# Optimization experiments

Hardware: AMD Instinct MI355X
Metric: run time of the kernel (lower is better)

The kernel has to match this reference:

```python
import jax, jax.numpy as jnp
import numpy as np

B, C, H, W, HEADS, S = 8, 512, 32, 32, 8, 77
CH = C // HEADS  # per-head channels = 64
GROUPS = 32      # GroupNorm32


def setup_inputs() -> dict:
    key = jax.random.key(0)
    ks = jax.random.split(key, 6)
    s = 0.02
    return {
        "x": jax.random.normal(ks[0], (B, C, H, W), jnp.float32),
        "encoder_out": jax.random.normal(ks[1], (B, C, S), jnp.float32),
        "capt_attn_mask": jax.random.bernoulli(ks[2], 0.9, (B, S)),
        "norm_scale": jnp.ones((C,), jnp.float32),
        "norm_bias": jnp.zeros((C,), jnp.float32),
        "qkv_w": jax.random.normal(ks[3], (3 * C, C), jnp.float32) * s,
        "qkv_b": jnp.zeros((3 * C,), jnp.float32),
        "ekv_w": jax.random.normal(ks[4], (2 * C, C), jnp.float32) * s,
        "ekv_b": jnp.zeros((2 * C,), jnp.float32),
        "proj_w": jax.random.normal(ks[5], (C, C), jnp.float32) * s,
        "proj_b": jnp.zeros((C,), jnp.float32),
    }


def reference(x, encoder_out, capt_attn_mask, norm_scale, norm_bias,
              qkv_w, qkv_b, ekv_w, ekv_b, proj_w, proj_b):
    b, c, h, w = x.shape
    T = h * w
    xf = x.reshape(b, c, T)

    # GroupNorm(32) in fp32 (GroupNorm32), affine
    xg = xf.reshape(b, GROUPS, c // GROUPS, T).astype(jnp.float32)
    mu = xg.mean(axis=(2, 3), keepdims=True)
    var = xg.var(axis=(2, 3), keepdims=True)
    nrm = ((xg - mu) * jax.lax.rsqrt(var + 1e-5)).reshape(b, c, T)
    nrm = nrm * norm_scale[None, :, None] + norm_bias[None, :, None]

    # 1x1 conv1d qkv projection: [b, 3c, T]
    qkv = jnp.einsum('oc,bct->bot', qkv_w, nrm) + qkv_b[None, :, None]
    qkv = qkv.reshape(b * HEADS, 3 * CH, T)
    q, k, v = jnp.split(qkv, 3, axis=1)  # each [b*heads, CH, T]

    # encoder kv: [b, 2c, S] -> [b*heads, 2*CH, S]
    ekv = jnp.einsum('oc,bcs->bos', ekv_w, encoder_out) + ekv_b[None, :, None]
    ekv = ekv.reshape(b * HEADS, 2 * CH, S)
    ek, ev = jnp.split(ekv, 2, axis=1)
    k = jnp.concatenate([ek, k], axis=-1)  # [b*heads, CH, S+T]
    v = jnp.concatenate([ev, v], axis=-1)

    scale = 1.0 / np.sqrt(np.sqrt(CH))
    wgt = jnp.einsum('bct,bcs->bts', q * scale, k * scale).astype(jnp.float32)

    # additive mask; torch.tile over dim0 is head-major (row i -> batch i % b),
    # faithfully reproduced; self-attn part (last T cols) is all-visible.
    addm_capt = jnp.where(jnp.tile(capt_attn_mask, (HEADS, 1)), 0.0, -10000.0)
    addm = jnp.concatenate(
        [addm_capt, jnp.zeros((b * HEADS, T), jnp.float32)], axis=1)[:, None, :]
    wgt = jax.nn.softmax(wgt + addm, axis=-1).astype(v.dtype)

    out = jnp.einsum('bts,bcs->bct', wgt, v)  # [b*heads, CH, T]
    out = out.reshape(b, c, T)
    out = jnp.einsum('oc,bct->bot', proj_w, out) + proj_b[None, :, None]
    return (xf + out).reshape(b, c, h, w)
```

## Files before the change

kernel.cpp:

```cpp
#include <hip/hip_runtime.h>
#include <math.h>

#define BB 8
#define TT 1024
#define SS 77

typedef short v8s __attribute__((ext_vector_type(8)));
typedef float v4f __attribute__((ext_vector_type(4)));
typedef unsigned short u16x4 __attribute__((ext_vector_type(4)));
typedef unsigned short u16x8 __attribute__((ext_vector_type(8)));
typedef unsigned short u16;

#define SCALEF 0.424660891f
#define MASKNEG (-14426.95f)

__device__ __forceinline__ u16 f2bf(float f) {
  unsigned u = __float_as_uint(f);
  u = (u + 0x7fffu + ((u >> 16) & 1u)) >> 16;
  return (u16)u;
}
__device__ __forceinline__ u16 hi16(float f) {
  return (u16)(__float_as_uint(f) >> 16);
}
__device__ __forceinline__ float bf2f(u16 u) {
  return __uint_as_float(((unsigned)u) << 16);
}
__device__ __forceinline__ void gl_lds16(const void* g, void* l) {
  __builtin_amdgcn_global_load_lds(
      (const __attribute__((address_space(1))) void*)g,
      (__attribute__((address_space(3))) void*)l, 16, 0, 0);
}

__global__ __launch_bounds__(256) void prep_gn_kernel(
    const float* __restrict__ x, const float* __restrict__ scale,
    const float* __restrict__ bias, u16* __restrict__ nrmT,
    const float* __restrict__ qkv_w, const float* __restrict__ ekv_w,
    const float* __restrict__ proj_w, const float* __restrict__ enc,
    const float* __restrict__ qkv_b, const float* __restrict__ ekv_b,
    u16* __restrict__ wQK, u16* __restrict__ wV, u16* __restrict__ wEK,
    u16* __restrict__ wEV, u16* __restrict__ projwb, u16* __restrict__ encT,
    float* __restrict__ bQK, float* __restrict__ bV,
    float* __restrict__ bEK, float* __restrict__ bEV) {
  __shared__ u16 Xs[16 * 1024];
  __shared__ float red[8];
  int blk = blockIdx.x, tid = threadIdx.x;

  if (blk < 256) {
    int bg = blk;
    int b = bg >> 5, g = bg & 31;
    const float4* x4 = (const float4*)(x + (size_t)bg * 16384);
    float s = 0.f, sq = 0.f;
#pragma unroll
    for (int i = 0; i < 16; ++i) {
      int idx = tid + 256 * i;
      float4 v = x4[idx];
      s += v.x + v.y + v.z + v.w;
      sq += v.x * v.x + v.y * v.y + v.z * v.z + v.w * v.w;
      int c = idx >> 8, t4 = (idx & 255) * 4;
      u16x4 o; o.x = f2bf(v.x); o.y = f2bf(v.y); o.z = f2bf(v.z); o.w = f2bf(v.w);
      *(u16x4*)(Xs + c * 1024 + t4) = o;
    }
#pragma unroll
    for (int off = 32; off > 0; off >>= 1) {
      s += __shfl_down(s, off, 64);
      sq += __shfl_down(sq, off, 64);
    }
    int wave = tid >> 6;
    if ((tid & 63) == 0) { red[wave] = s; red[wave + 4] = sq; }
    __syncthreads();
    float ts = red[0] + red[1] + red[2] + red[3];
    float tq = red[4] + red[5] + red[6] + red[7];
    float mu = ts * (1.0f / 16384.0f);
    float var = tq * (1.0f / 16384.0f) - mu * mu;
    float rs = rsqrtf(var + 1e-5f);
    float scv[16], biv[16];
#pragma unroll
    for (int c = 0; c < 16; ++c) {
      float ss = scale[g * 16 + c] * rs;
      scv[c] = ss;
      biv[c] = bias[g * 16 + c] - mu * ss;
    }
#pragma unroll
    for (int j = 0; j < 4; ++j) {
      int t = tid + 256 * j;
      u16x8 o0, o1;
#pragma unroll
      for (int c = 0; c < 8; ++c)  o0[c] = f2bf(bf2f(Xs[c * 1024 + t]) * scv[c] + biv[c]);
#pragma unroll
      for (int c = 8; c < 16; ++c) o1[c - 8] = f2bf(bf2f(Xs[c * 1024 + t]) * scv[c] + biv[c]);
      u16* dst = nrmT + ((size_t)b * 1024 + t) * 512 + g * 16;
      *(u16x8*)dst = o0;
      *(u16x8*)(dst + 8) = o1;
    }
    return;
  }

  int p = blk - 256;
  if (p < 512) {
    int idx = p * 256 + tid;
    int n = idx >> 7, c4 = (idx & 127) * 4;
    int which = n >> 9, h = (n >> 6) & 7, ch = n & 63;
    int src = h * 192 + which * 64 + ch;
    float4 v = *(const float4*)(qkv_w + (size_t)src * 512 + c4);
    u16x4 o; o.x = f2bf(v.x * SCALEF); o.y = f2bf(v.y * SCALEF);
    o.z = f2bf(v.z * SCALEF); o.w = f2bf(v.w * SCALEF);
    *(u16x4*)(wQK + (size_t)n * 512 + c4) = o;
  } else if (p < 768) {
    int idx = (p - 512) * 256 + tid;
    int n = idx >> 7, c4 = (idx & 127) * 4;
    int h = n >> 6, ch = n & 63;
    int src = h * 192 + 128 + ch;
    float4 v = *(const float4*)(qkv_w + (size_t)src * 512 + c4);
    u16x4 o; o.x = f2bf(v.x); o.y = f2bf(v.y); o.z = f2bf(v.z); o.w = f2bf(v.w);
    *(u16x4*)(wV + (size_t)n * 512 + c4) = o;
  } else if (p < 1024) {
    int idx = (p - 768) * 256 + tid;
    int n = idx >> 7, c4 = (idx & 127) * 4;
    int h = n >> 6, ch = n & 63;
    int src = h * 128 + ch;
    float4 v = *(const float4*)(ekv_w + (size_t)src * 512 + c4);
    u16x4 o; o.x = f2bf(v.x * SCALEF); o.y = f2bf(v.y * SCALEF);
    o.z = f2bf(v.z * SCALEF); o.w = f2bf(v.w * SCALEF);
    *(u16x4*)(wEK + (size_t)n * 512 + c4) = o;
  } else if (p < 1280) {
    int idx = (p - 1024) * 256 + tid;
    int n = idx >> 7, c4 = (idx & 127) * 4;
    int h = n >> 6, ch = n & 63;
    int src = h * 128 + 64 + ch;
    float4 v = *(const float4*)(ekv_w + (size_t)src * 512 + c4);
    u16x4 o; o.x = f2bf(v.x); o.y = f2bf(v.y); o.z = f2bf(v.z); o.w = f2bf(v.w);
    *(u16x4*)(wEV + (size_t)n * 512 + c4) = o;
  } else if (p < 1536) {
    int idx = (p - 1280) * 256 + tid;
    float4 v = ((const float4*)proj_w)[idx];
    u16x4 o; o.x = f2bf(v.x); o.y = f2bf(v.y); o.z = f2bf(v.z); o.w = f2bf(v.w);
    *(u16x4*)(projwb + (size_t)idx * 4) = o;
  } else if (p < 2048) {
    int idx = (p - 1536) * 256 + tid;
    int b = idx >> 14, rem = idx & 16383;
    int s = rem >> 7, c = (rem & 127) * 4;
    u16x4 o; o.x = 0; o.y = 0; o.z = 0; o.w = 0;
    if (s < SS) {
      const float* pp = enc + ((size_t)b * 512 + c) * SS + s;
      o.x = f2bf(pp[0]); o.y = f2bf(pp[SS]); o.z = f2bf(pp[2 * SS]); o.w = f2bf(pp[3 * SS]);
    }
    *(u16x4*)(encT + ((size_t)b * 128 + s) * 512 + c) = o;
  } else {
    for (int i = tid; i < 2560; i += 256) {
      if (i < 1024) {
        int which = i >> 9, h = (i >> 6) & 7, ch = i & 63;
        bQK[i] = qkv_b[h * 192 + which * 64 + ch] * SCALEF;
      } else if (i < 1536) {
        int j = i - 1024; int h = j >> 6, ch = j & 63;
        bV[j] = qkv_b[h * 192 + 128 + ch];
      } else if (i < 2048) {
        int j = i - 1536; int h = j >> 6, ch = j & 63;
        bEK[j] = ekv_b[h * 128 + ch] * SCALEF;
      } else {
        int j = i - 2048; int h = j >> 6, ch = j & 63;
        bEV[j] = ekv_b[h * 128 + 64 + ch];
      }
    }
  }
}

__global__ __launch_bounds__(256) void proj_all(
    const u16* __restrict__ nrmT, const u16* __restrict__ encT,
    const u16* __restrict__ wQK, const u16* __restrict__ wEK,
    const u16* __restrict__ wV, const u16* __restrict__ wEV,
    const float* __restrict__ bQK, const float* __restrict__ bEK,
    const float* __restrict__ bV, const float* __restrict__ bEV,
    u16* __restrict__ Qh, u16* __restrict__ Kfull, u16* __restrict__ Vfull) {
  __shared__ __align__(16) u16 SH[16384];
  u16* As = SH;
  u16* Bs = SH + 8192;

  int job = blockIdx.x, bz = blockIdx.y;
  int tid = threadIdx.x;
  int lane = tid & 63, w = tid >> 6;
  int lan15 = lane & 15, quad = lane >> 4;
  int wm = w >> 1, wn = w & 1;

  int mode, m0, n0;
  const u16 *Ap, *Bp;
  const float* bias;
  u16 *dA = nullptr, *dB = nullptr;
  int TrA = 0, offA = 0, TrB = 0, offB = 0;
  int coff = 0;

  if (job < 64) {
    mode = 3; m0 = (job >> 3) * 128; n0 = (job & 7) * 128;
    Ap = nrmT + (size_t)bz * 1024 * 512; Bp = wQK; bias = bQK;
    dA = Qh; TrA = 1024; offA = 0; dB = Kfull; TrB = 1152; offB = 128;
  } else if (job < 68) {
    mode = 3; m0 = 0; n0 = (job - 64) * 128;
    Ap = encT + (size_t)bz * 128 * 512; Bp = wEK; bias = bEK;
    dA = Kfull; TrA = 1152; offA = 0; dB = Kfull; TrB = 1152; offB = 0;
  } else if (job < 100) {
    int jj = job - 68; mode = 0; m0 = (jj >> 3) * 128; n0 = (jj & 7) * 128;
    Ap = wV; Bp = nrmT + (size_t)bz * 1024 * 512; bias = bV;
    coff = 128;
  } else {
    int jj = job - 100; mode = 0; m0 = jj * 128; n0 = 0;
    Ap = wEV; Bp = encT + (size_t)bz * 128 * 512; bias = bEV;
    coff = 0;
  }

  int srow = lane >> 3;
  int schunk = (lane & 7) ^ srow;
  const char* Ag = (const char*)(Ap + (size_t)(m0 + w * 32 + srow) * 512) + schunk * 16;
  const char* Bg = (const char*)(Bp + (size_t)(n0 + w * 32 + srow) * 512) + schunk * 16;
  char* Al = (char*)As + w * 4096;
  char* Bl = (char*)Bs + w * 4096;

  v4f acc[4][4] = {};

  for (int step = 0; step < 8; ++step) {
    __syncthreads();
    int kb = step * 128;
#pragma unroll
    for (int i = 0; i < 4; ++i) gl_lds16(Ag + kb + i * 8192, Al + i * 1024);
#pragma unroll
    for (int i = 0; i < 4; ++i) gl_lds16(Bg + kb + i * 8192, Bl + i * 1024);
    __syncthreads();

#pragma unroll
    for (int ksub = 0; ksub < 2; ++ksub) {
      int ch = ((ksub * 4 + quad) ^ (lan15 & 7)) * 16;
      v8s a[4], bf[4];
#pragma unroll
      for (int i = 0; i < 4; ++i)
        a[i] = *(const v8s*)((const char*)As + (wm * 64 + i * 16 + lan15) * 128 + ch);
#pragma unroll
      for (int j = 0; j < 4; ++j)
        bf[j] = *(const v8s*)((const char*)Bs + (wn * 64 + j * 16 + lan15) * 128 + ch);
#pragma unroll
      for (int i = 0; i < 4; ++i)
#pragma unroll
        for (int j = 0; j < 4; ++j)
          acc[i][j] = __builtin_amdgcn_mfma_f32_16x16x32_bf16(a[i], bf[j], acc[i][j], 0, 0, 0);
    }
  }

  if (mode == 3) {
    u16* Tr = SH;
    for (int ph = 0; ph < 2; ++ph) {
      __syncthreads();
      if (wn == ph) {
#pragma unroll
        for (int j = 0; j < 4; ++j) {
          int n = n0 + wn * 64 + j * 16 + lan15;
          float bv_ = bias[n];
#pragma unroll
          for (int i = 0; i < 4; ++i)
#pragma unroll
            for (int r = 0; r < 4; ++r)
              Tr[(wm * 64 + i * 16 + quad * 4 + r) * 72 + j * 16 + lan15] =
                  f2bf(acc[i][j][r] + bv_);
        }
      }
      __syncthreads();
      int nb = n0 + ph * 64;
      u16* dst = (nb < 512) ? dA : dB;
      int Trows = (nb < 512) ? TrA : TrB;
      int roff  = (nb < 512) ? offA : offB;
      int hh = (nb & 511) >> 6;
      int row = tid >> 1, seg = (tid & 1) * 32;
      u16* dp = dst + ((size_t)(bz * 8 + hh) * Trows + roff + m0 + row) * 64 + seg;
#pragma unroll
      for (int g = 0; g < 4; ++g)
        *(u16x8*)(dp + g * 8) = *(const u16x8*)(Tr + row * 72 + seg + g * 8);
    }
  } else {
    u16* Tr = SH;
    u16* Cb = Vfull + (size_t)bz * 512 * 1152;
    for (int ph = 0; ph < 2; ++ph) {
      __syncthreads();
      if (wn == ph) {
#pragma unroll
        for (int i = 0; i < 4; ++i) {
          int ob = wm * 64 + i * 16 + quad * 4;
#pragma unroll
          for (int r = 0; r < 4; ++r) {
            float bi = bias[m0 + ob + r];
#pragma unroll
            for (int j = 0; j < 4; ++j)
              Tr[(ob + r) * 72 + j * 16 + lan15] = f2bf(acc[i][j][r] + bi);
          }
        }
      }
      __syncthreads();
      int row = tid >> 1, seg = (tid & 1) * 32;
      u16* dp = Cb + (size_t)(m0 + row) * 1152 + coff + n0 + ph * 64 + seg;
#pragma unroll
      for (int g = 0; g < 4; ++g)
        *(u16x8*)(dp + g * 8) = *(const u16x8*)(Tr + row * 72 + seg + g * 8);
    }
  }
}

__global__ __launch_bounds__(256) void proj_out(
    const u16* __restrict__ A, const u16* __restrict__ B,
    const float* __restrict__ bias, const float* __restrict__ res,
    float* __restrict__ Cf) {
  __shared__ __align__(16) u16 SH[16384];
  u16* As = SH;
  u16* Bs = SH + 8192;

  int tid = threadIdx.x;
  int lane = tid & 63, w = tid >> 6;
  int lan15 = lane & 15, quad = lane >> 4;
  int wm = w >> 1, wn = w & 1;
  int m0 = blockIdx.y * 128, n0 = blockIdx.x * 128;
  int bz = blockIdx.z;
  const u16* Bb = B + (size_t)bz * 1024 * 512;

  int srow = lane >> 3;
  int schunk = (lane & 7) ^ srow;
  const char* Ag = (const char*)(A + (size_t)(m0 + w * 32 + srow) * 512) + schunk * 16;
  const char* Bg = (const char*)(Bb + (size_t)(n0 + w * 32 + srow) * 512) + schunk * 16;
  char* Al = (char*)As + w * 4096;
  char* Bl = (char*)Bs + w * 4096;

  v4f acc[4][4] = {};

  for (int step = 0; step < 8; ++step) {
    __syncthreads();
    int kb = step * 128;
#pragma unroll
    for (int i = 0; i < 4; ++i) gl_lds16(Ag + kb + i * 8192, Al + i * 1024);
#pragma unroll
    for (int i = 0; i < 4; ++i) gl_lds16(Bg + kb + i * 8192, Bl + i * 1024);
    __syncthreads();

#pragma unroll
    for (int ksub = 0; ksub < 2; ++ksub) {
      int ch = ((ksub * 4 + quad) ^ (lan15 & 7)) * 16;
      v8s a[4], bf[4];
#pragma unroll
      for (int i = 0; i < 4; ++i)
        a[i] = *(const v8s*)((const char*)As + (wm * 64 + i * 16 + lan15) * 128 + ch);
#pragma unroll
      for (int j = 0; j < 4; ++j)
        bf[j] = *(const v8s*)((const char*)Bs + (wn * 64 + j * 16 + lan15) * 128 + ch);
#pragma unroll
      for (int i = 0; i < 4; ++i)
#pragma unroll
        for (int j = 0; j < 4; ++j)
          acc[i][j] = __builtin_amdgcn_mfma_f32_16x16x32_bf16(a[i], bf[j], acc[i][j], 0, 0, 0);
    }
  }

  const float* rb = res + (size_t)bz * 512 * 1024;
  float* Cb = Cf + (size_t)bz * 512 * 1024;
#pragma unroll
  for (int i = 0; i < 4; ++i) {
    int ob = m0 + wm * 64 + i * 16 + quad * 4;
#pragma unroll
    for (int r = 0; r < 4; ++r) {
      int o = ob + r;
      float bi = bias[o];
#pragma unroll
      for (int j = 0; j < 4; ++j) {
        int n = n0 + wn * 64 + j * 16 + lan15;
        Cb[(size_t)o * 1024 + n] = acc[i][j][r] + bi + rb[(size_t)o * 1024 + n];
      }
    }
  }
}

#define AOFF_K 0
#define AOFF_V 24576
#define AOFF_P 49152
#define AOFF_AM 67584
#define ASMEM  68096

__global__ __launch_bounds__(512, 4) void attn_kernel(
    const u16* __restrict__ Qh, const u16* __restrict__ Kf,
    const u16* __restrict__ Vf, const int* __restrict__ mask,
    u16* __restrict__ attnT) {
  __shared__ __align__(16) unsigned char smem[ASMEM];
  float* AM = (float*)(smem + AOFF_AM);

  int bh = blockIdx.x, b = bh >> 3, h = bh & 7;
  int t0 = blockIdx.y * 128;
  int tid = threadIdx.x;
  int lane = tid & 63, w = tid >> 6;
  int lan15 = lane & 15, quad = lane >> 4;
  int r8 = lane >> 3, c8 = lane & 7;
  int swE = (c8 ^ r8) * 8;

  const u16* Qb = Qh + (size_t)bh * 1024 * 64;
  const u16* Kb = Kf + (size_t)bh * 1152 * 64;
  const u16* Vb = Vf + (size_t)bh * 64 * 1152;
  char* Pw = (char*)smem + AOFF_P + w * 2304;
  u16* Pu = (u16*)Pw;

  if (tid < 128)
    AM[tid] = (tid < SS) ? ((mask[h * SS + tid] != 0) ? 0.f : MASKNEG) : -1e30f;

#pragma unroll
  for (int i = 0; i < 2; ++i)
    gl_lds16(Qb + (size_t)(t0 + w * 16 + i * 8 + r8) * 64 + swE, Pw + i * 1024);
#pragma unroll
  for (int cc = 0; cc < 2; ++cc) {
    int row = w * 8;
    gl_lds16(Kb + (size_t)(cc * 64 + row + r8) * 64 + swE,
             (char*)smem + AOFF_K + cc * 8192 + row * 128);
    gl_lds16(Vb + (size_t)(row + r8) * 1152 + cc * 64 + swE,
             (char*)smem + AOFF_V + cc * 8192 + row * 128);
  }

  asm volatile("s_waitcnt vmcnt(4)" ::: "memory");
  __builtin_amdgcn_sched_barrier(0);

  v8s aq[2];
#pragma unroll
  for (int ks = 0; ks < 2; ++ks)
    aq[ks] = *(const v8s*)(Pw + lan15 * 128 +
                           (((ks * 4 + quad) ^ (lan15 & 7)) * 16));

  asm volatile("s_waitcnt vmcnt(2) lgkmcnt(0)" ::: "memory");
  __builtin_amdgcn_sched_barrier(0);
  __builtin_amdgcn_s_barrier();
  __builtin_amdgcn_sched_barrier(0);

  v4f O[4] = {};
  float lsum = 0.f;
  int cur = 0;

  for (int c = 0; c < 18; ++c) {
    if (c < 16) {
      int nb = cur + 2; if (nb >= 3) nb -= 3;
      int row = w * 8;
      gl_lds16(Kb + (size_t)((c + 2) * 64 + row + r8) * 64 + swE,
               (char*)smem + AOFF_K + nb * 8192 + row * 128);
      gl_lds16(Vb + (size_t)(row + r8) * 1152 + (c + 2) * 64 + swE,
               (char*)smem + AOFF_V + nb * 8192 + row * 128);
    }
    const char* Kc = (const char*)smem + AOFF_K + cur * 8192;
    const char* Vc = (const char*)smem + AOFF_V + cur * 8192;

    v4f ST[4] = {};
#pragma unroll
    for (int ks = 0; ks < 2; ++ks) {
      int cofs = ((ks * 4 + quad) ^ (lan15 & 7)) * 16;
      v8s bk[4];
#pragma unroll
      for (int nt = 0; nt < 4; ++nt)
        bk[nt] = *(const v8s*)(Kc + (nt * 16 + lan15) * 128 + cofs);
      __builtin_amdgcn_s_setprio(1);
#pragma unroll
      for (int nt = 0; nt < 4; ++nt)
        ST[nt] = __builtin_amdgcn_mfma_f32_16x16x32_bf16(bk[nt], aq[ks], ST[nt], 0, 0, 0);
      __builtin_amdgcn_s_setprio(0);
    }

    if (c < 2) {
#pragma unroll
      for (int nt = 0; nt < 4; ++nt)
#pragma unroll
        for (int r = 0; r < 4; ++r)
          ST[nt][r] += AM[c * 64 + nt * 16 + quad * 4 + r];
    }

#pragma unroll
    for (int nt = 0; nt < 4; ++nt) {
      float e0 = __builtin_amdgcn_exp2f(ST[nt][0]);
      float e1 = __builtin_amdgcn_exp2f(ST[nt][1]);
      float e2 = __builtin_amdgcn_exp2f(ST[nt][2]);
      float e3 = __builtin_amdgcn_exp2f(ST[nt][3]);
      u16x4 pk; pk.x = hi16(e0); pk.y = hi16(e1); pk.z = hi16(e2); pk.w = hi16(e3);
      *(u16x4*)&Pu[lan15 * 72 + nt * 16 + quad * 4] = pk;
      lsum += (e0 + e1) + (e2 + e3);
    }

#pragma unroll
    for (int ks = 0; ks < 2; ++ks) {
      int cofs = ((ks * 4 + quad) ^ (lan15 & 7)) * 16;
      v8s ap, bv[4];
      ap = *(const v8s*)(Pw + lan15 * 144 + ks * 64 + quad * 16);
#pragma unroll
      for (int nc = 0; nc < 4; ++nc)
        bv[nc] = *(const v8s*)(Vc + (nc * 16 + lan15) * 128 + cofs);
      __builtin_amdgcn_s_setprio(1);
#pragma unroll
      for (int nc = 0; nc < 4; ++nc)
        O[nc] = __builtin_amdgcn_mfma_f32_16x16x32_bf16(ap, bv[nc], O[nc], 0, 0, 0);
      __builtin_amdgcn_s_setprio(0);
    }

    if (c < 17) {
      if (c < 16) asm volatile("s_waitcnt vmcnt(2)" ::: "memory");
      else        asm volatile("s_waitcnt vmcnt(0)" ::: "memory");
      __builtin_amdgcn_sched_barrier(0);
      __builtin_amdgcn_s_barrier();
      __builtin_amdgcn_sched_barrier(0);
    }
    cur = cur + 1; if (cur == 3) cur = 0;
  }

  {
    float v = lsum;
    v += __shfl_xor(v, 16, 64);
    v += __shfl_xor(v, 32, 64);
    AM[w * 16 + lan15] = v;
  }
  __syncthreads();
  float inv[4];
#pragma unroll
  for (int r = 0; r < 4; ++r)
    inv[r] = 1.0f / AM[w * 16 + quad * 4 + r];

  float* Ot = (float*)smem;
#pragma unroll
  for (int nc = 0; nc < 4; ++nc)
#pragma unroll
    for (int r = 0; r < 4; ++r)
      Ot[(w * 16 + quad * 4 + r) * 68 + nc * 16 + lan15] = O[nc][r] * inv[r];
  __syncthreads();
  {
    int row = tid >> 2, seg = (tid & 3) * 16;
    const float* src = Ot + row * 68 + seg;
    u16* dp = attnT + ((size_t)b * 1024 + t0 + row) * 512 + h * 64 + seg;
#pragma unroll
    for (int g = 0; g < 2; ++g) {
      u16x8 o;
#pragma unroll
      for (int k = 0; k < 8; ++k) o[k] = f2bf(src[g * 8 + k]);
      *(u16x8*)(dp + g * 8) = o;
    }
  }
}

extern "C" void kernel_launch(void* const* d_in, const int* in_sizes, int n_in,
                              void* d_out, int out_size, void* d_ws, size_t ws_size,
                              hipStream_t stream) {
  const float* x       = (const float*)d_in[0];
  const float* enc     = (const float*)d_in[1];
  const int*   mask    = (const int*)d_in[2];
  const float* nscale  = (const float*)d_in[3];
  const float* nbias   = (const float*)d_in[4];
  const float* qkv_w   = (const float*)d_in[5];
  const float* qkv_b   = (const float*)d_in[6];
  const float* ekv_w   = (const float*)d_in[7];
  const float* ekv_b   = (const float*)d_in[8];
  const float* proj_w  = (const float*)d_in[9];
  const float* proj_b  = (const float*)d_in[10];
  float* out = (float*)d_out;

  char* ws = (char*)d_ws;
  const size_t MiB = 1048576;
  u16* nrmT   = (u16*)(ws);
  u16* Qh     = (u16*)(ws + 8 * MiB);
  u16* Kfull  = (u16*)(ws + 16 * MiB);
  u16* Vfull  = (u16*)(ws + 26 * MiB);
  u16* attnT  = (u16*)(ws + 36 * MiB);
  u16* encT   = (u16*)(ws + 44 * MiB);
  u16* wQK    = (u16*)(ws + 45 * MiB);
  u16* wV     = (u16*)(ws + 46 * MiB);
  u16* wEK    = (u16*)(ws + 46 * MiB + 524288);
  u16* wEV    = (u16*)(ws + 47 * MiB);
  u16* projwb = (u16*)(ws + 47 * MiB + 524288);
  float* bQK  = (float*)(ws + 48 * MiB);
  float* bV   = (float*)(ws + 48 * MiB + 4096);
  float* bEK  = (float*)(ws + 48 * MiB + 6144);
  float* bEV  = (float*)(ws + 48 * MiB + 8192);

  prep_gn_kernel<<<dim3(2305), dim3(256), 0, stream>>>(
      x, nscale, nbias, nrmT, qkv_w, ekv_w, proj_w, enc, qkv_b, ekv_b,
      wQK, wV, wEK, wEV, projwb, encT, bQK, bV, bEK, bEV);

  proj_all<<<dim3(104, BB), dim3(256), 0, stream>>>(
      nrmT, encT, wQK, wEK, wV, wEV, bQK, bEK, bV, bEV, Qh, Kfull, Vfull);

  attn_kernel<<<dim3(64, 8), dim3(512), 0, stream>>>(
      Qh, Kfull, Vfull, mask, attnT);

  proj_out<<<dim3(8, 4, BB), dim3(256), 0, stream>>>(
      projwb, attnT, proj_b, x, out);
}
```

Measured before the change: 172.5 us.

## Fuse projection, attention and output GEMMs into one persistent kernel with grid barriers

Merges the QKV projection, attention and output projection launches into a single 512-block, 512-thread persistent kernel. Two software grid barriers, built from atomic counters reset by the prep kernel, separate the phases. The aim is to cut launch gaps and tail effects between the three kernels. In exchange the projection GEMM tiles shrink (each wave now covers a 64x32 tile, and the output GEMM uses smaller tiles). Correctness depends on all 512 blocks being co-resident, otherwise the spin barrier deadlocks.

```diff
diff --git a/kernel.cpp b/kernel.cpp
--- a/kernel.cpp
+++ b/kernel.cpp
@@ -4,6 +4,7 @@
 #define BB 8
 #define TT 1024
 #define SS 77
+#define NBLK 512u
 
 typedef short v8s __attribute__((ext_vector_type(8)));
 typedef float v4f __attribute__((ext_vector_type(4)));
@@ -29,6 +30,19 @@
   __builtin_amdgcn_global_load_lds(
       (const __attribute__((address_space(1))) void*)g,
       (__attribute__((address_space(3))) void*)l, 16, 0, 0);
+}
+
+__device__ __forceinline__ void grid_sync(unsigned* bar, int slot) {
+  __syncthreads();
+  if (threadIdx.x == 0) {
+    __threadfence();
+    unsigned* c = bar + slot * 32;
+    atomicAdd(c, 1u);
+    while (__hip_atomic_load(c, __ATOMIC_RELAXED, __HIP_MEMORY_SCOPE_AGENT) < NBLK)
+      __builtin_amdgcn_s_sleep(2);
+    __threadfence();
+  }
+  __syncthreads();
 }
 
 __global__ __launch_bounds__(256) void prep_gn_kernel(
@@ -40,7 +54,8 @@
     u16* __restrict__ wQK, u16* __restrict__ wV, u16* __restrict__ wEK,
     u16* __restrict__ wEV, u16* __restrict__ projwb, u16* __restrict__ encT,
     float* __restrict__ bQK, float* __restrict__ bV,
-    float* __restrict__ bEK, float* __restrict__ bEV) {
+    float* __restrict__ bEK, float* __restrict__ bEV,
+    unsigned* __restrict__ bar) {
   __shared__ u16 Xs[16 * 1024];
   __shared__ float red[8];
   int blk = blockIdx.x, tid = threadIdx.x;
@@ -146,6 +161,7 @@
     }
     *(u16x4*)(encT + ((size_t)b * 128 + s) * 512 + c) = o;
   } else {
+    if (tid < 64) bar[tid] = 0;
     for (int i = tid; i < 2560; i += 256) {
       if (i < 1024) {
         int which = i >> 9, h = (i >> 6) & 7, ch = i & 63;
@@ -164,371 +180,354 @@
   }
 }
 
-__global__ __launch_bounds__(256) void proj_all(
+#define AOFF_K 0
+#define AOFF_V 24576
+#define AOFF_P 49152
+#define AOFF_AM 67584
+#define ASMEM  68096
+
+__global__ __launch_bounds__(512, 4) void mega_kernel(
     const u16* __restrict__ nrmT, const u16* __restrict__ encT,
     const u16* __restrict__ wQK, const u16* __restrict__ wEK,
     const u16* __restrict__ wV, const u16* __restrict__ wEV,
     const float* __restrict__ bQK, const float* __restrict__ bEK,
     const float* __restrict__ bV, const float* __restrict__ bEV,
-    u16* __restrict__ Qh, u16* __restrict__ Kfull, u16* __restrict__ Vfull) {
-  __shared__ __align__(16) u16 SH[16384];
-  u16* As = SH;
-  u16* Bs = SH + 8192;
-
-  int job = blockIdx.x, bz = blockIdx.y;
-  int tid = threadIdx.x;
+    u16* __restrict__ Qh, u16* __restrict__ Kfull, u16* __restrict__ Vfull,
+    const int* __restrict__ mask, u16* __restrict__ attnT,
+    const u16* __restrict__ projwb, const float* __restrict__ proj_b,
+    const float* __restrict__ xres, float* __restrict__ out,
+    unsigned* __restrict__ bar) {
+  __shared__ __align__(16) unsigned char smem[ASMEM];
+  int blk = blockIdx.x, tid = threadIdx.x;
   int lane = tid & 63, w = tid >> 6;
   int lan15 = lane & 15, quad = lane >> 4;
-  int wm = w >> 1, wn = w & 1;
-
-  int mode, m0, n0;
-  const u16 *Ap, *Bp;
-  const float* bias;
-  u16 *dA = nullptr, *dB = nullptr;
-  int TrA = 0, offA = 0, TrB = 0, offB = 0;
-  int coff = 0;
-
-  if (job < 64) {
-    mode = 3; m0 = (job >> 3) * 128; n0 = (job & 7) * 128;
-    Ap = nrmT + (size_t)bz * 1024 * 512; Bp = wQK; bias = bQK;
-    dA = Qh; TrA = 1024; offA = 0; dB = Kfull; TrB = 1152; offB = 128;
-  } else if (job < 68) {
-    mode = 3; m0 = 0; n0 = (job - 64) * 128;
-    Ap = encT + (size_t)bz * 128 * 512; Bp = wEK; bias = bEK;
-    dA = Kfull; TrA = 1152; offA = 0; dB = Kfull; TrB = 1152; offB = 0;
-  } else if (job < 100) {
-    int jj = job - 68; mode = 0; m0 = (jj >> 3) * 128; n0 = (jj & 7) * 128;
-    Ap = wV; Bp = nrmT + (size_t)bz * 1024 * 512; bias = bV;
-    coff = 128;
-  } else {
-    int jj = job - 100; mode = 0; m0 = jj * 128; n0 = 0;
-    Ap = wEV; Bp = encT + (size_t)bz * 128 * 512; bias = bEV;
-    coff = 0;
+  int srow = lane >> 3, c8 = lane & 7;
+  int schunk = c8 ^ srow;
+
+  {
+    u16* As = (u16*)smem;
+    u16* Bs = (u16*)(smem + 16384);
+    int wm = w >> 2, wn = w & 3;
+
+    for (int jid = blk; jid < 832; jid += 512) {
+      int bz = jid / 104, job = jid - bz * 104;
+      int mode, m0, n0;
+      const u16 *Ap, *Bp;
+      const float* bias;
+      u16 *dA = nullptr, *dB = nullptr;
+      int TrA = 0, offA = 0, TrB = 0, offB = 0, coff = 0;
+
+      if (job < 64) {
+        mode = 3; m0 = (job >> 3) * 128; n0 = (job & 7) * 128;
+        Ap = nrmT + (size_t)bz * 1024 * 512; Bp = wQK; bias = bQK;
+        dA = Qh; TrA = 1024; offA = 0; dB = Kfull; TrB = 1152; offB = 128;
+      } else if (job < 68) {
+        mode = 3; m0 = 0; n0 = (job - 64) * 128;
+        Ap = encT + (size_t)bz * 128 * 512; Bp = wEK; bias = bEK;
+        dA = Kfull; TrA = 1152; offA = 0; dB = Kfull; TrB = 1152; offB = 0;
+      } else if (job < 100) {
+        int jj = job - 68; mode = 0; m0 = (jj >> 3) * 128; n0 = (jj & 7) * 128;
+        Ap = wV; Bp = nrmT + (size_t)bz * 1024 * 512; bias = bV;
+        coff = 128;
+      } else {
+        int jj = job - 100; mode = 0; m0 = jj * 128; n0 = 0;
+        Ap = wEV; Bp = encT + (size_t)bz * 128 * 512; bias = bEV;
+        coff = 0;
+      }
+
+      const char* Ag = (const char*)(Ap + (size_t)(m0 + w * 16 + srow) * 512) + schunk * 16;
+      const char* Bg = (const char*)(Bp + (size_t)(n0 + w * 16 + srow) * 512) + schunk * 16;
+      char* Al = (char*)As + w * 2048;
+      char* Bl = (char*)Bs + w * 2048;
+
+      v4f acc[4][2] = {};
+
+      for (int step = 0; step < 8; ++step) {
+        __syncthreads();
+        int kb = step * 128;
+#pragma unroll
+        for (int i = 0; i < 2; ++i) gl_lds16(Ag + kb + i * 8192, Al + i * 1024);
+#pragma unroll
+        for (int i = 0; i < 2; ++i) gl_lds16(Bg + kb + i * 8192, Bl + i * 1024);
+        __syncthreads();
+
+#pragma unroll
+        for (int ksub = 0; ksub < 2; ++ksub) {
+          int ch = ((ksub * 4 + quad) ^ (lan15 & 7)) * 16;
+          v8s a[4], bf[2];
+#pragma unroll
+          for (int i = 0; i < 4; ++i)
+            a[i] = *(const v8s*)((const char*)As + (wm * 64 + i * 16 + lan15) * 128 + ch);
+#pragma unroll
+          for (int j = 0; j < 2; ++j)
+            bf[j] = *(const v8s*)((const char*)Bs + (wn * 32 + j * 16 + lan15) * 128 + ch);
+#pragma unroll
+          for (int i = 0; i < 4; ++i)
+#pragma unroll
+            for (int j = 0; j < 2; ++j)
+              acc[i][j] = __builtin_amdgcn_mfma_f32_16x16x32_bf16(a[i], bf[j], acc[i][j], 0, 0, 0);
+        }
+      }
+
+      u16* Tr = (u16*)smem;
+      if (mode == 3) {
+        for (int ph = 0; ph < 2; ++ph) {
+          __syncthreads();
+          if ((wn >> 1) == ph) {
+#pragma unroll
+            for (int j = 0; j < 2; ++j) {
+              int n = n0 + wn * 32 + j * 16 + lan15;
+              float bv_ = bias[n];
+#pragma unroll
+              for (int i = 0; i < 4; ++i)
+#pragma unroll
+                for (int r = 0; r < 4; ++r)
+                  Tr[(wm * 64 + i * 16 + quad * 4 + r) * 72 + (wn & 1) * 32 + j * 16 + lan15] =
+                      f2bf(acc[i][j][r] + bv_);
+            }
+          }
+          __syncthreads();
+          int nb = n0 + ph * 64;
+          u16* dst = (nb < 512) ? dA : dB;
+          int Trows = (nb < 512) ? TrA : TrB;
+          int roff  = (nb < 512) ? offA : offB;
+          int hh = (nb & 511) >> 6;
+          int row = tid >> 2, seg = (tid & 3) * 16;
+          u16* dp = dst + ((size_t)(bz * 8 + hh) * Trows + roff + m0 + row) * 64 + seg;
+#pragma unroll
+          for (int g = 0; g < 2; ++g)
+            *(u16x8*)(dp + g * 8) = *(const u16x8*)(Tr + row * 72 + seg + g * 8);
+        }
+      } else {
+        u16* Cb = Vfull + (size_t)bz * 512 * 1152;
+        for (int ph = 0; ph < 2; ++ph) {
+          __syncthreads();
+          if ((wn >> 1) == ph) {
+#pragma unroll
+            for (int i = 0; i < 4; ++i) {
+              int ob = wm * 64 + i * 16 + quad * 4;
+#pragma unroll
+              for (int r = 0; r < 4; ++r) {
+                float bi = bias[m0 + ob + r];
+#pragma unroll
+                for (int j = 0; j < 2; ++j)
+                  Tr[(ob + r) * 72 + (wn & 1) * 32 + j * 16 + lan15] = f2bf(acc[i][j][r] + bi);
+              }
+            }
+          }
+          __syncthreads();
+          int row = tid >> 2, seg = (tid & 3) * 16;
+          u16* dp = Cb + (size_t)(m0 + row) * 1152 + coff + n0 + ph * 64 + seg;
+#pragma unroll
+          for (int g = 0; g < 2; ++g)
+            *(u16x8*)(dp + g * 8) = *(const u16x8*)(Tr + row * 72 + seg + g * 8);
+        }
+      }
+    }
   }
 
-  int srow = lane >> 3;
-  int schunk = (lane & 7) ^ srow;
-  const char* Ag = (const char*)(Ap + (size_t)(m0 + w * 32 + srow) * 512) + schunk * 16;
-  const char* Bg = (const char*)(Bp + (size_t)(n0 + w * 32 + srow) * 512) + schunk * 16;
-  char* Al = (char*)As + w * 4096;
-  char* Bl = (char*)Bs + w * 4096;
-
-  v4f acc[4][4] = {};
-
-  for (int step = 0; step < 8; ++step) {
+  grid_sync(bar, 0);
+
+  {
+    float* AM = (float*)(smem + AOFF_AM);
+    int bh = blk & 63, b = bh >> 3, h = bh & 7;
+    int t0 = (blk >> 6) * 128;
+    int r8 = srow;
+    int swE = schunk * 8;
+
+    const u16* Qb = Qh + (size_t)bh * 1024 * 64;
+    const u16* Kb = Kfull + (size_t)bh * 1152 * 64;
+    const u16* Vb = Vfull + (size_t)bh * 64 * 1152;
+    char* Pw = (char*)smem + AOFF_P + w * 2304;
+    u16* Pu = (u16*)Pw;
+
+    if (tid < 128)
+      AM[tid] = (tid < SS) ? ((mask[h * SS + tid] != 0) ? 0.f : MASKNEG) : -1e30f;
+
+#pragma unroll
+    for (int i = 0; i < 2; ++i)
+      gl_lds16(Qb + (size_t)(t0 + w * 16 + i * 8 + r8) * 64 + swE, Pw + i * 1024);
+#pragma unroll
+    for (int cc = 0; cc < 2; ++cc) {
+      int row = w * 8;
+      gl_lds16(Kb + (size_t)(cc * 64 + row + r8) * 64 + swE,
+               (char*)smem + AOFF_K + cc * 8192 + row * 128);
+      gl_lds16(Vb + (size_t)(row + r8) * 1152 + cc * 64 + swE,
+               (char*)smem + AOFF_V + cc * 8192 + row * 128);
+    }
+
+    asm volatile("s_waitcnt vmcnt(4)" ::: "memory");
+    __builtin_amdgcn_sched_barrier(0);
+
+    v8s aq[2];
+#pragma unroll
+    for (int ks = 0; ks < 2; ++ks)
+      aq[ks] = *(const v8s*)(Pw + lan15 * 128 +
+                             (((ks * 4 + quad) ^ (lan15 & 7)) * 16));
+
+    asm volatile("s_waitcnt vmcnt(2) lgkmcnt(0)" ::: "memory");
+    __builtin_amdgcn_sched_barrier(0);
+    __builtin_amdgcn_s_barrier();
+    __builtin_amdgcn_sched_barrier(0);
+
+    v4f O[4] = {};
+    float lsum = 0.f;
+    int cur = 0;
+
+    for (int c = 0; c < 18; ++c) {
+      if (c < 16) {
+        int nb = cur + 2; if (nb >= 3) nb -= 3;
+        int row = w * 8;
+        gl_lds16(Kb + (size_t)((c + 2) * 64 + row + r8) * 64 + swE,
+                 (char*)smem + AOFF_K + nb * 8192 + row * 128);
+        gl_lds16(Vb + (size_t)(row + r8) * 1152 + (c + 2) * 64 + swE,
+                 (char*)smem + AOFF_V + nb * 8192 + row * 128);
+      }
+      const char* Kc = (const char*)smem + AOFF_K + cur * 8192;
+      const char* Vc = (const char*)smem + AOFF_V + cur * 8192;
+
+      v4f ST[4] = {};
+#pragma unroll
+      for (int ks = 0; ks < 2; ++ks) {
+        int cofs = ((ks * 4 + quad) ^ (lan15 & 7)) * 16;
+        v8s bk[4];
+#pragma unroll
+        for (int nt = 0; nt < 4; ++nt)
+          bk[nt] = *(const v8s*)(Kc + (nt * 16 + lan15) * 128 + cofs);
+        __builtin_amdgcn_s_setprio(1);
+#pragma unroll
+        for (int nt = 0; nt < 4; ++nt)
+          ST[nt] = __builtin_amdgcn_mfma_f32_16x16x32_bf16(bk[nt], aq[ks], ST[nt], 0, 0, 0);
+        __builtin_amdgcn_s_setprio(0);
+      }
+
+      if (c < 2) {
+#pragma unroll
+        for (int nt = 0; nt < 4; ++nt)
+#pragma unroll
+          for (int r = 0; r < 4; ++r)
+            ST[nt][r] += AM[c * 64 + nt * 16 + quad * 4 + r];
+      }
+
+#pragma unroll
+      for (int nt = 0; nt < 4; ++nt) {
+        float e0 = __builtin_amdgcn_exp2f(ST[nt][0]);
+        float e1 = __builtin_amdgcn_exp2f(ST[nt][1]);
+        float e2 = __builtin_amdgcn_exp2f(ST[nt][2]);
+        float e3 = __builtin_amdgcn_exp2f(ST[nt][3]);
+        u16x4 pk; pk.x = hi16(e0); pk.y = hi16(e1); pk.z = hi16(e2); pk.w = hi16(e3);
+        *(u16x4*)&Pu[lan15 * 72 + nt * 16 + quad * 4] = pk;
+        lsum += (e0 + e1) + (e2 + e3);
+      }
+
+#pragma unroll
+      for (int ks = 0; ks < 2; ++ks) {
+        int cofs = ((ks * 4 + quad) ^ (lan15 & 7)) * 16;
+        v8s ap, bv[4];
+        ap = *(const v8s*)(Pw + lan15 * 144 + ks * 64 + quad * 16);
+#pragma unroll
+        for (int nc = 0; nc < 4; ++nc)
+          bv[nc] = *(const v8s*)(Vc + (nc * 16 + lan15) * 128 + cofs);
+        __builtin_amdgcn_s_setprio(1);
+#pragma unroll
+        for (int nc = 0; nc < 4; ++nc)
+          O[nc] = __builtin_amdgcn_mfma_f32_16x16x32_bf16(ap, bv[nc], O[nc], 0, 0, 0);
+        __builtin_amdgcn_s_setprio(0);
+      }
+
+      if (c < 17) {
+        if (c < 16) asm volatile("s_waitcnt vmcnt(2)" ::: "memory");
+        else        asm volatile("s_waitcnt vmcnt(0)" ::: "memory");
+        __builtin_amdgcn_sched_barrier(0);
+        __builtin_amdgcn_s_barrier();
+        __builtin_amdgcn_sched_barrier(0);
+      }
+      cur = cur + 1; if (cur == 3) cur = 0;
+    }
+
+    {
+      float v = lsum;
+      v += __shfl_xor(v, 16, 64);
+      v += __shfl_xor(v, 32, 64);
+      AM[w * 16 + lan15] = v;
+    }
     __syncthreads();
-    int kb = step * 128;
-#pragma unroll
-    for (int i = 0; i < 4; ++i) gl_lds16(Ag + kb + i * 8192, Al + i * 1024);
-#pragma unroll
-    for (int i = 0; i < 4; ++i) gl_lds16(Bg + kb + i * 8192, Bl + i * 1024);
+    float inv[4];
+#pragma unroll
+    for (int r = 0; r < 4; ++r)
+      inv[r] = 1.0f / AM[w * 16 + quad * 4 + r];
+
+    float* Ot = (float*)smem;
+#pragma unroll
+    for (int nc = 0; nc < 4; ++nc)
+#pragma unroll
+      for (int r = 0; r < 4; ++r)
+        Ot[(w * 16 + quad * 4 + r) * 68 + nc * 16 + lan15] = O[nc][r] * inv[r];
     __syncthreads();
-
-#pragma unroll
-    for (int ksub = 0; ksub < 2; ++ksub) {
-      int ch = ((ksub * 4 + quad) ^ (lan15 & 7)) * 16;
-      v8s a[4], bf[4];
-#pragma unroll
-      for (int i = 0; i < 4; ++i)
-        a[i] = *(const v8s*)((const char*)As + (wm * 64 + i * 16 + lan15) * 128 + ch);
-#pragma unroll
-      for (int j = 0; j < 4; ++j)
-        bf[j] = *(const v8s*)((const char*)Bs + (wn * 64 + j * 16 + lan15) * 128 + ch);
-#pragma unroll
-      for (int i = 0; i < 4; ++i)
-#pragma unroll
-        for (int j = 0; j < 4; ++j)
-          acc[i][j] = __builtin_amdgcn_mfma_f32_16x16x32_bf16(a[i], bf[j], acc[i][j], 0, 0, 0);
+    {
+      int row = tid >> 2, seg = (tid & 3) * 16;
+      const float* src = Ot + row * 68 + seg;
+      u16* dp = attnT + ((size_t)b * 1024 + t0 + row) * 512 + h * 64 + seg;
+#pragma unroll
+      for (int g = 0; g < 2; ++g) {
+        u16x8 o;
+#pragma unroll
+        for (int k = 0; k < 8; ++k) o[k] = f2bf(src[g * 8 + k]);
+        *(u16x8*)(dp + g * 8) = o;
+      }
     }
   }
 
-  if (mode == 3) {
-    u16* Tr = SH;
-    for (int ph = 0; ph < 2; ++ph) {
+  grid_sync(bar, 1);
+
+  {
+    u16* As = (u16*)smem;
+    u16* Bs = (u16*)(smem + 8192);
+    int bz = blk >> 6, r_ = blk & 63;
+    int m0 = (r_ >> 3) * 64, n0 = (r_ & 7) * 128;
+    const u16* Bb = attnT + (size_t)bz * 1024 * 512;
+
+    const char* Ag = (const char*)(projwb + (size_t)(m0 + w * 8 + srow) * 512) + schunk * 16;
+    const char* Bg = (const char*)(Bb + (size_t)(n0 + w * 16 + srow) * 512) + schunk * 16;
+    char* Al = (char*)As + w * 1024;
+    char* Bl = (char*)Bs + w * 2048;
+
+    v4f acc[4] = {};
+
+    for (int step = 0; step < 8; ++step) {
       __syncthreads();
-      if (wn == ph) {
-#pragma unroll
-        for (int j = 0; j < 4; ++j) {
-          int n = n0 + wn * 64 + j * 16 + lan15;
-          float bv_ = bias[n];
-#pragma unroll
-          for (int i = 0; i < 4; ++i)
-#pragma unroll
-            for (int r = 0; r < 4; ++r)
-              Tr[(wm * 64 + i * 16 + quad * 4 + r) * 72 + j * 16 + lan15] =
-                  f2bf(acc[i][j][r] + bv_);
-        }
-      }
+      int kb = step * 128;
+      gl_lds16(Ag + kb, Al);
+#pragma unroll
+      for (int i = 0; i < 2; ++i) gl_lds16(Bg + kb + i * 8192, Bl + i * 1024);
       __syncthreads();
-      int nb = n0 + ph * 64;
-      u16* dst = (nb < 512) ? dA : dB;
-      int Trows = (nb < 512) ? TrA : TrB;
-      int roff  = (nb < 512) ? offA : offB;
-      int hh = (nb & 511) >> 6;
-      int row = tid >> 1, seg = (tid & 1) * 32;
-      u16* dp = dst + ((size_t)(bz * 8 + hh) * Trows + roff + m0 + row) * 64 + seg;
-#pragma unroll
-      for (int g = 0; g < 4; ++g)
-        *(u16x8*)(dp + g * 8) = *(const u16x8*)(Tr + row * 72 + seg + g * 8);
-    }
-  } else {
-    u16* Tr = SH;
-    u16* Cb = Vfull + (size_t)bz * 512 * 1152;
-    for (int ph = 0; ph < 2; ++ph) {
-      __syncthreads();
-      if (wn == ph) {
-#pragma unroll
-        for (int i = 0; i < 4; ++i) {
-          int ob = wm * 64 + i * 16 + quad * 4;
-#pragma unroll
-          for (int r = 0; r < 4; ++r) {
-            float bi = bias[m0 + ob + r];
-#pragma unroll
-            for (int j = 0; j < 4; ++j)
-              Tr[(ob + r) * 72 + j * 16 + lan15] = f2bf(acc[i][j][r] + bi);
-          }
-        }
-      }
-      __syncthreads();
-      int row = tid >> 1, seg = (tid & 1) * 32;
-      u16* dp = Cb + (size_t)(m0 + row) * 1152 + coff + n0 + ph * 64 + seg;
-#pragma unroll
-      for (int g = 0; g < 4; ++g)
-        *(u16x8*)(dp + g * 8) = *(const u16x8*)(Tr + row * 72 + seg + g * 8);
-    }
-  }
-}
-
-__global__ __launch_bounds__(256) void proj_out(
-    const u16* __restrict__ A, const u16* __restrict__ B,
-    const float* __restrict__ bias, const float* __restrict__ res,
-    float* __restrict__ Cf) {
-  __shared__ __align__(16) u16 SH[16384];
-  u16* As = SH;
-  u16* Bs = SH + 8192;
-
-  int tid = threadIdx.x;
-  int lane = tid & 63, w = tid >> 6;
-  int lan15 = lane & 15, quad = lane >> 4;
-  int wm = w >> 1, wn = w & 1;
-  int m0 = blockIdx.y * 128, n0 = blockIdx.x * 128;
-  int bz = blockIdx.z;
-  const u16* Bb = B + (size_t)bz * 1024 * 512;
-
-  int srow = lane >> 3;
-  int schunk = (lane & 7) ^ srow;
-  const char* Ag = (const char*)(A + (size_t)(m0 + w * 32 + srow) * 512) + schunk * 16;
-  const char* Bg = (const char*)(Bb + (size_t)(n0 + w * 32 + srow) * 512) + schunk * 16;
-  char* Al = (char*)As + w * 4096;
-  char* Bl = (char*)Bs + w * 4096;
-
-  v4f acc[4][4] = {};
-
-  for (int step = 0; step < 8; ++step) {
-    __syncthreads();
-    int kb = step * 128;
-#pragma unroll
-    for (int i = 0; i < 4; ++i) gl_lds16(Ag + kb + i * 8192, Al + i * 1024);
-#pragma unroll
-    for (int i = 0; i < 4; ++i) gl_lds16(Bg + kb + i * 8192, Bl + i * 1024);
-    __syncthreads();
-
-#pragma unroll
-    for (int ksub = 0; ksub < 2; ++ksub) {
-      int ch = ((ksub * 4 + quad) ^ (lan15 & 7)) * 16;
-      v8s a[4], bf[4];
-#pragma unroll
-      for (int i = 0; i < 4; ++i)
-        a[i] = *(const v8s*)((const char*)As + (wm * 64 + i * 16 + lan15) * 128 + ch);
-#pragma unroll
-      for (int j = 0; j < 4; ++j)
-        bf[j] = *(const v8s*)((const char*)Bs + (wn * 64 + j * 16 + lan15) * 128 + ch);
-#pragma unroll
-      for (int i = 0; i < 4; ++i)
-#pragma unroll
-        for (int j = 0; j < 4; ++j)
-          acc[i][j] = __builtin_amdgcn_mfma_f32_16x16x32_bf16(a[i], bf[j], acc[i][j], 0, 0, 0);
-    }
-  }
-
-  const float* rb = res + (size_t)bz * 512 * 1024;
-  float* Cb = Cf + (size_t)bz * 512 * 1024;
-#pragma unroll
-  for (int i = 0; i < 4; ++i) {
-    int ob = m0 + wm * 64 + i * 16 + quad * 4;
-#pragma unroll
-    for (int r = 0; r < 4; ++r) {
-      int o = ob + r;
-      float bi = bias[o];
-#pragma unroll
-      for (int j = 0; j < 4; ++j) {
-        int n = n0 + wn * 64 + j * 16 + lan15;
-        Cb[(size_t)o * 1024 + n] = acc[i][j][r] + bi + rb[(size_t)o * 1024 + n];
-      }
-    }
-  }
-}
-
-#define AOFF_K 0
-#define AOFF_V 24576
-#define AOFF_P 49152
-#define AOFF_AM 67584
-#define ASMEM  68096
-
-__global__ __launch_bounds__(512, 4) void attn_kernel(
-    const u16* __restrict__ Qh, const u16* __restrict__ Kf,
-    const u16* __restrict__ Vf, const int* __restrict__ mask,
-    u16* __restrict__ attnT) {
-  __shared__ __align__(16) unsigned char smem[ASMEM];
-  float* AM = (float*)(smem + AOFF_AM);
-
-  int bh = blockIdx.x, b = bh >> 3, h = bh & 7;
-  int t0 = blockIdx.y * 128;
-  int tid = threadIdx.x;
-  int lane = tid & 63, w = tid >> 6;
-  int lan15 = lane & 15, quad = lane >> 4;
-  int r8 = lane >> 3, c8 = lane & 7;
-  int swE = (c8 ^ r8) * 8;
-
-  const u16* Qb = Qh + (size_t)bh * 1024 * 64;
-  const u16* Kb = Kf + (size_t)bh * 1152 * 64;
-  const u16* Vb = Vf + (size_t)bh * 64 * 1152;
-  char* Pw = (char*)smem + AOFF_P + w * 2304;
-  u16* Pu = (u16*)Pw;
-
-  if (tid < 128)
-    AM[tid] = (tid < SS) ? ((mask[h * SS + tid] != 0) ? 0.f : MASKNEG) : -1e30f;
-
-#pragma unroll
-  for (int i = 0; i < 2; ++i)
-    gl_lds16(Qb + (size_t)(t0 + w * 16 + i * 8 + r8) * 64 + swE, Pw + i * 1024);
-#pragma unroll
-  for (int cc = 0; cc < 2; ++cc) {
-    int row = w * 8;
-    gl_lds16(Kb + (size_t)(cc * 64 + row + r8) * 64 + swE,
-             (char*)smem + AOFF_K + cc * 8192 + row * 128);
-    gl_lds16(Vb + (size_t)(row + r8) * 1152 + cc * 64 + swE,
-             (char*)smem + AOFF_V + cc * 8192 + row * 128);
-  }
-
-  asm volatile("s_waitcnt vmcnt(4)" ::: "memory");
-  __builtin_amdgcn_sched_barrier(0);
-
-  v8s aq[2];
-#pragma unroll
-  for (int ks = 0; ks < 2; ++ks)
-    aq[ks] = *(const v8s*)(Pw + lan15 * 128 +
-                           (((ks * 4 + quad) ^ (lan15 & 7)) * 16));
-
-  asm volatile("s_waitcnt vmcnt(2) lgkmcnt(0)" ::: "memory");
-  __builtin_amdgcn_sched_barrier(0);
-  __builtin_amdgcn_s_barrier();
-  __builtin_amdgcn_sched_barrier(0);
-
-  v4f O[4] = {};
-  float lsum = 0.f;
-  int cur = 0;
-
-  for (int c = 0; c < 18; ++c) {
-    if (c < 16) {
-      int nb = cur + 2; if (nb >= 3) nb -= 3;
-      int row = w * 8;
-      gl_lds16(Kb + (size_t)((c + 2) * 64 + row + r8) * 64 + swE,
-               (char*)smem + AOFF_K + nb * 8192 + row * 128);
-      gl_lds16(Vb + (size_t)(row + r8) * 1152 + (c + 2) * 64 + swE,
-               (char*)smem + AOFF_V + nb * 8192 + row * 128);
-    }
-    const char* Kc = (const char*)smem + AOFF_K + cur * 8192;
-    const char* Vc = (const char*)smem + AOFF_V + cur * 8192;
-
-    v4f ST[4] = {};
-#pragma unroll
-    for (int ks = 0; ks < 2; ++ks) {
-      int cofs = ((ks * 4 + quad) ^ (lan15 & 7)) * 16;
-      v8s bk[4];
-#pragma unroll
-      for (int nt = 0; nt < 4; ++nt)
-        bk[nt] = *(const v8s*)(Kc + (nt * 16 + lan15) * 128 + cofs);
-      __builtin_amdgcn_s_setprio(1);
-#pragma unroll
-      for (int nt = 0; nt < 4; ++nt)
-        ST[nt] = __builtin_amdgcn_mfma_f32_16x16x32_bf16(bk[nt], aq[ks], ST[nt], 0, 0, 0);
-      __builtin_amdgcn_s_setprio(0);
-    }
-
-    if (c < 2) {
-#pragma unroll
-      for (int nt = 0; nt < 4; ++nt)
-#pragma unroll
-        for (int r = 0; r < 4; ++r)
-          ST[nt][r] += AM[c * 64 + nt * 16 + quad * 4 + r];
-    }
-
-#pragma unroll
-    for (int nt = 0; nt < 4; ++nt) {
-      float e0 = __builtin_amdgcn_exp2f(ST[nt][0]);
-      float e1 = __builtin_amdgcn_exp2f(ST[nt][1]);
-      float e2 = __builtin_amdgcn_exp2f(ST[nt][2]);
-      float e3 = __builtin_amdgcn_exp2f(ST[nt][3]);
-      u16x4 pk; pk.x = hi16(e0); pk.y = hi16(e1); pk.z = hi16(e2); pk.w = hi16(e3);
-      *(u16x4*)&Pu[lan15 * 72 + nt * 16 + quad * 4] = pk;
-      lsum += (e0 + e1) + (e2 + e3);
-    }
-
-#pragma unroll
-    for (int ks = 0; ks < 2; ++ks) {
-      int cofs = ((ks * 4 + quad) ^ (lan15 & 7)) * 16;
-      v8s ap, bv[4];
-      ap = *(const v8s*)(Pw + lan15 * 144 + ks * 64 + quad * 16);
-#pragma unroll
-      for (int nc = 0; nc < 4; ++nc)
-        bv[nc] = *(const v8s*)(Vc + (nc * 16 + lan15) * 128 + cofs);
-      __builtin_amdgcn_s_setprio(1);
-#pragma unroll
-      for (int nc = 0; nc < 4; ++nc)
-        O[nc] = __builtin_amdgcn_mfma_f32_16x16x32_bf16(ap, bv[nc], O[nc], 0, 0, 0);
-      __builtin_amdgcn_s_setprio(0);
-    }
-
-    if (c < 17) {
-      if (c < 16) asm volatile("s_waitcnt vmcnt(2)" ::: "memory");
-      else        asm volatile("s_waitcnt vmcnt(0)" ::: "memory");
-      __builtin_amdgcn_sched_barrier(0);
-      __builtin_amdgcn_s_barrier();
-      __builtin_amdgcn_sched_barrier(0);
-    }
-    cur = cur + 1; if (cur == 3) cur = 0;
-  }
-
-  {
-    float v = lsum;
-    v += __shfl_xor(v, 16, 64);
-    v += __shfl_xor(v, 32, 64);
-    AM[w * 16 + lan15] = v;
-  }
-  __syncthreads();
-  float inv[4];
-#pragma unroll
-  for (int r = 0; r < 4; ++r)
-    inv[r] = 1.0f / AM[w * 16 + quad * 4 + r];
-
-  float* Ot = (float*)smem;
-#pragma unroll
-  for (int nc = 0; nc < 4; ++nc)
-#pragma unroll
-    for (int r = 0; r < 4; ++r)
-      Ot[(w * 16 + quad * 4 + r) * 68 + nc * 16 + lan15] = O[nc][r] * inv[r];
-  __syncthreads();
-  {
-    int row = tid >> 2, seg = (tid & 3) * 16;
-    const float* src = Ot + row * 68 + seg;
-    u16* dp = attnT + ((size_t)b * 1024 + t0 + row) * 512 + h * 64 + seg;
-#pragma unroll
-    for (int g = 0; g < 2; ++g) {
-      u16x8 o;
-#pragma unroll
-      for (int k = 0; k < 8; ++k) o[k] = f2bf(src[g * 8 + k]);
-      *(u16x8*)(dp + g * 8) = o;
+
+#pragma unroll
+      for (int ksub = 0; ksub < 2; ++ksub) {
+        int ch = ((ksub * 4 + quad) ^ (lan15 & 7)) * 16;
+        v8s a[4], bv;
+#pragma unroll
+        for (int i = 0; i < 4; ++i)
+          a[i] = *(const v8s*)((const char*)As + (i * 16 + lan15) * 128 + ch);
+        bv = *(const v8s*)((const char*)Bs + (w * 16 + lan15) * 128 + ch);
+#pragma unroll
+        for (int i = 0; i < 4; ++i)
+          acc[i] = __builtin_amdgcn_mfma_f32_16x16x32_bf16(a[i], bv, acc[i], 0, 0, 0);
+      }
+    }
+
+    const float* rb = xres + (size_t)bz * 512 * 1024;
+    float* Cb = out + (size_t)bz * 512 * 1024;
+#pragma unroll
+    for (int i = 0; i < 4; ++i) {
+      int ob = m0 + i * 16 + quad * 4;
+#pragma unroll
+      for (int rr = 0; rr < 4; ++rr) {
+        int o = ob + rr;
+        float bi = proj_b[o];
+        int n = n0 + w * 16 + lan15;
+        Cb[(size_t)o * 1024 + n] = acc[i][rr] + bi + rb[(size_t)o * 1024 + n];
+      }
     }
   }
 }
@@ -566,17 +565,13 @@
   float* bV   = (float*)(ws + 48 * MiB + 4096);
   float* bEK  = (float*)(ws + 48 * MiB + 6144);
   float* bEV  = (float*)(ws + 48 * MiB + 8192);
+  unsigned* bar = (unsigned*)(ws + 50 * MiB);
 
   prep_gn_kernel<<<dim3(2305), dim3(256), 0, stream>>>(
       x, nscale, nbias, nrmT, qkv_w, ekv_w, proj_w, enc, qkv_b, ekv_b,
-      wQK, wV, wEK, wEV, projwb, encT, bQK, bV, bEK, bEV);
-
-  proj_all<<<dim3(104, BB), dim3(256), 0, stream>>>(
-      nrmT, encT, wQK, wEK, wV, wEV, bQK, bEK, bV, bEV, Qh, Kfull, Vfull);
-
-  attn_kernel<<<dim3(64, 8), dim3(512), 0, stream>>>(
-      Qh, Kfull, Vfull, mask, attnT);
-
-  proj_out<<<dim3(8, 4, BB), dim3(256), 0, stream>>>(
-      projwb, attnT, proj_b, x, out);
-}
+      wQK, wV, wEK, wEV, projwb, encT, bQK, bV, bEK, bEV, bar);
+
+  mega_kernel<<<dim3(512), dim3(512), 0, stream>>>(
+      nrmT, encT, wQK, wEK, wV, wEV, bQK, bEK, bV, bEV,
+      Qh, Kfull, Vfull, mask, attnT, projwb, proj_b, x, out, bar);
+}
```

New measurement: 272.7 us. 1.58x slower.
